# Kernel tuning notes

Measured on AMD Instinct MI355X. Metric: run time of the kernel, lower is better.

## Reference

```python
import jax, jax.numpy as jnp
import numpy as np
from jax import lax

L, B, D = 512, 128, 512   # listener frames, batch, listener feature dim
T, E, C, H, V = 200, 384, 128, 512, 46  # decode steps, embed, context, hidden(=E+C), vocab


def setup_inputs() -> dict:
    key = jax.random.key(0)
    ks = jax.random.split(key, 32)
    def p(i, shape, s=0.02):
        return jax.random.normal(ks[i], shape, dtype=jnp.float32) * s
    return {
        "listener_features": jax.random.normal(ks[0], (L, B, D), dtype=jnp.float32),
        "utterance_lengths": jax.random.randint(ks[1], (B,), L // 2, L + 1),
        "transcript": jax.random.randint(ks[2], (T, B), 0, V),
        "embedding": p(3, (V, E), 1.0),
        "w_ih0": p(4, (4 * H, E + C)), "w_hh0": p(5, (4 * H, H)),
        "b_ih0": jnp.zeros((4 * H,), jnp.float32), "b_hh0": jnp.zeros((4 * H,), jnp.float32),
        "w_ih1": p(6, (4 * H, H)), "w_hh1": p(7, (4 * H, H)),
        "b_ih1": jnp.zeros((4 * H,), jnp.float32), "b_hh1": jnp.zeros((4 * H,), jnp.float32),
        "w_ih2": p(8, (4 * H, H)), "w_hh2": p(9, (4 * H, H)),
        "b_ih2": jnp.zeros((4 * H,), jnp.float32), "b_hh2": jnp.zeros((4 * H,), jnp.float32),
        "phi_w": p(10, (C, H)), "phi_b": jnp.zeros((C,), jnp.float32),
        "key_w": p(11, (C, D)), "key_b": jnp.zeros((C,), jnp.float32),
        "value_w": p(12, (C, D)), "value_b": jnp.zeros((C,), jnp.float32),
        "out_w": p(13, (V, H + C)), "out_b": jnp.zeros((V,), jnp.float32),
        "init_hx0": jnp.zeros((1, H), jnp.float32), "init_cx0": jnp.zeros((1, H), jnp.float32),
        "init_hx1": jnp.zeros((1, H), jnp.float32), "init_cx1": jnp.zeros((1, H), jnp.float32),
        "init_hx2": jnp.zeros((1, H), jnp.float32), "init_cx2": jnp.zeros((1, H), jnp.float32),
    }


def _lstm_cell(x, h, c, w_ih, w_hh, b_ih, b_hh):
    gates = x @ w_ih.T + b_ih + h @ w_hh.T + b_hh  # [B,4H]
    i, f, g, o = jnp.split(gates, 4, axis=-1)
    c2 = jax.nn.sigmoid(f) * c + jax.nn.sigmoid(i) * jnp.tanh(g)
    h2 = jax.nn.sigmoid(o) * jnp.tanh(c2)
    return h2, c2


def reference(listener_features, utterance_lengths, transcript, embedding,
              w_ih0, w_hh0, b_ih0, b_hh0, w_ih1, w_hh1, b_ih1, b_hh1,
              w_ih2, w_hh2, b_ih2, b_hh2, phi_w, phi_b, key_w, key_b,
              value_w, value_b, out_w, out_b,
              init_hx0, init_cx0, init_hx1, init_cx1, init_hx2, init_cx2):
    nL, nB = listener_features.shape[0], listener_features.shape[1]
    mask = (jnp.arange(nL)[None, :] < utterance_lengths[:, None]).astype(jnp.float32)  # [B,L]
    # key/value projections are step-invariant (original recomputes them each step; same math)
    keyf = jnp.einsum('lbd,cd->blc', listener_features, key_w) + key_b   # [B,L,C]
    valf = jnp.einsum('lbd,cd->blc', listener_features, value_w) + value_b  # [B,L,C]

    def attend(hx2):
        q = hx2 @ phi_w.T + phi_b                      # [B,C]
        energy = jnp.einsum('bc,blc->bl', q, keyf)     # [B,L]
        a = jax.nn.softmax(energy, axis=-1) * mask
        a = a / jnp.maximum(jnp.sum(a, axis=-1, keepdims=True), 1e-12)  # F.normalize(p=1)
        ctx = jnp.einsum('bl,blc->bc', a, valf)        # [B,C]
        return a, ctx

    hx0 = jnp.broadcast_to(init_hx0, (nB, H)); cx0 = jnp.broadcast_to(init_cx0, (nB, H))
    hx1 = jnp.broadcast_to(init_hx1, (nB, H)); cx1 = jnp.broadcast_to(init_cx1, (nB, H))
    hx2 = jnp.broadcast_to(init_hx2, (nB, H)); cx2 = jnp.broadcast_to(init_cx2, (nB, H))
    _, ctx = attend(hx2)  # initial context from initial decoder state

    # teacher forcing: step t consumes <sos>(=0) then transcript[t-1]
    in_chars = jnp.concatenate([jnp.zeros((1, nB), transcript.dtype), transcript[:-1]], axis=0)  # [T,B]
    emb = embedding[in_chars]  # [T,B,E]

    def step(carry, emb_t):
        hx0, cx0, hx1, cx1, hx2, cx2, ctx = carry
        x = jnp.concatenate([emb_t, ctx], axis=-1)  # [B,E+C]
        hx0, cx0 = _lstm_cell(x, hx0, cx0, w_ih0, w_hh0, b_ih0, b_hh0)
        hx1, cx1 = _lstm_cell(hx0, hx1, cx1, w_ih1, w_hh1, b_ih1, b_hh1)
        hx2, cx2 = _lstm_cell(hx1, hx2, cx2, w_ih2, w_hh2, b_ih2, b_hh2)
        a, ctx = attend(hx2)
        logits = jnp.concatenate([hx2, ctx], axis=-1) @ out_w.T + out_b  # [B,V]
        return (hx0, cx0, hx1, cx1, hx2, cx2, ctx), (logits, a)

    carry0 = (hx0, cx0, hx1, cx1, hx2, cx2, ctx)
    _, (logits, attn) = lax.scan(step, carry0, emb)
    return logits, attn  # [T,B,V], [T,B,L]
```

## Files before the change

### kernel.cpp

```cpp
#include <hip/hip_runtime.h>

typedef unsigned short UST;
typedef unsigned int uint32;
typedef float f32x4 __attribute__((ext_vector_type(4)));
typedef short s16x8 __attribute__((ext_vector_type(8)));


__device__ __forceinline__ float b2f(UST u) {
  uint32 x = ((uint32)u) << 16;
  union { uint32 u; float f; } v; v.u = x; return v.f;
}
__device__ __forceinline__ UST f2bf(float f) {
  union { float f; uint32 u; } v; v.f = f;
  uint32 r = (v.u + 0x7fffu + ((v.u >> 16) & 1u)) >> 16;
  return (UST)r;
}
__device__ __forceinline__ ushort4 f2bf4(float4 v) {
  ushort4 r; r.x = f2bf(v.x); r.y = f2bf(v.y); r.z = f2bf(v.z); r.w = f2bf(v.w); return r;
}
__device__ __forceinline__ float sigf(float x) { return 1.f / (1.f + __expf(-x)); }
__device__ __forceinline__ float tanhf_(float x) { return 2.f / (1.f + __expf(-2.f * x)) - 1.f; }

union U8 { unsigned long long u; ushort4 s; uint2 w; };

__device__ __forceinline__ void st_flag(int* p, int v) {
  __hip_atomic_store(p, v, __ATOMIC_RELAXED, __HIP_MEMORY_SCOPE_AGENT);
}
__device__ __forceinline__ int ld_flag(const int* p) {
  return __hip_atomic_load(p, __ATOMIC_RELAXED, __HIP_MEMORY_SCOPE_AGENT);
}
__device__ __forceinline__ unsigned long long ld8(const void* p) {
  return __hip_atomic_load((const unsigned long long*)p, __ATOMIC_RELAXED, __HIP_MEMORY_SCOPE_AGENT);
}
__device__ __forceinline__ void st4(void* p, uint32 v) {
  __hip_atomic_store((uint32*)p, v, __ATOMIC_RELAXED, __HIP_MEMORY_SCOPE_AGENT);
}
__device__ __forceinline__ uint4 ld16c(const UST* p) {
  U8 a, b; a.u = ld8(p); b.u = ld8(p + 4);
  uint4 v; v.x = a.w.x; v.y = a.w.y; v.z = b.w.x; v.w = b.w.y; return v;
}

__device__ __forceinline__ void signal_flag(int* fl, int idx, int val, int tid) {
  __atomic_signal_fence(__ATOMIC_SEQ_CST);
  __builtin_amdgcn_s_waitcnt(0);
  __atomic_signal_fence(__ATOMIC_SEQ_CST);
  __syncthreads();
  if (tid == 0) st_flag(&fl[idx * 16], val);
}
__device__ __forceinline__ void wait128f(int* fl, int val, int tid, unsigned long long dl) {
  if (tid < 128) {
    while (ld_flag(&fl[tid * 16]) < val) {
      if (__builtin_amdgcn_s_memrealtime() > dl) break;
      __builtin_amdgcn_s_sleep(1);
    }
  }
  __syncthreads();
}
__device__ __forceinline__ void wait64f(int* fl, int val, int tid, unsigned long long dl) {
  if (tid < 64) {
    while (ld_flag(&fl[tid * 16]) < val) {
      if (__builtin_amdgcn_s_memrealtime() > dl) break;
      __builtin_amdgcn_s_sleep(1);
    }
  }
  __syncthreads();
}

struct Args {
  const float* lf; const int* ulen; const int* tr; const float* emb;
  const float* wih0; const float* whh0; const float* bih0; const float* bhh0;
  const float* wih1; const float* whh1; const float* bih1; const float* bhh1;
  const float* wih2; const float* whh2; const float* bih2; const float* bhh2;
  const float* phi_w; const float* phi_b; const float* key_w; const float* key_b;
  const float* val_w; const float* val_b; const float* out_w; const float* out_b;
  const float* ihx0; const float* icx0; const float* ihx1; const float* icx1;
  const float* ihx2; const float* icx2;
  int* bar; UST* wr; UST* xemb; UST* phi_bf; UST* keyfT; UST* valfT;
  UST* hx0; UST* hx1; UST* hx2; UST* ctx; UST* h2h; UST* cxh;
  float* out_logits; float* out_attn;
};

__global__ void __launch_bounds__(256) kprep(Args A) {
  const long N0 = 8192;
  const long N1 = 3L * 2048 * 1024;
  const long N2 = 200L * 128 * 384;
  const long N3 = 128L * 512;
  long total = N0 + N1 + N2 + N3;
  long stride = (long)gridDim.x * blockDim.x;
  for (long ii = (long)blockIdx.x * 256 + threadIdx.x; ii < total; ii += stride) {
    long j = ii;
    if (j < N0) { A.bar[j] = 0; continue; }
    j -= N0;
    if (j < N1) {
      int q = (int)j;
      int i = q & 7, lane = (q >> 3) & 63, nt = (q >> 9) & 1, ks = (q >> 10) & 31;
      int js = (q >> 15) & 63, cell = q >> 21;
      int gr = js * 32 + nt * 16 + (lane & 15);
      int jc = gr >> 2, g = gr & 3, k = ks * 32 + (lane >> 4) * 8 + i;
      const float* wi = cell == 0 ? A.wih0 : cell == 1 ? A.wih1 : A.wih2;
      const float* wh = cell == 0 ? A.whh0 : cell == 1 ? A.whh1 : A.whh2;
      float v;
      if (cell == 0)
        v = (k < 384) ? wi[(g * 512 + jc) * 512 + k]
          : (k < 896) ? wh[(g * 512 + jc) * 512 + k - 384]
                      : wi[(g * 512 + jc) * 512 + k - 512];
      else
        v = (k < 512) ? wi[(g * 512 + jc) * 512 + k] : wh[(g * 512 + jc) * 512 + k - 512];
      A.wr[j] = f2bf(v);
      continue;
    }
    j -= N1;
    if (j < N2) {
      int t = (int)(j / 49152); int r = (int)(j % 49152); int bb = r / 384; int e = r - bb * 384;
      int ch = (t == 0) ? 0 : A.tr[(t - 1) * 128 + bb];
      A.xemb[j] = f2bf(A.emb[ch * 384 + e]);
      continue;
    }
    j -= N2;
    A.phi_bf[j] = f2bf(A.phi_w[j]);
  }
}

__global__ void __launch_bounds__(256) kkv(Args A) {
  __shared__ __attribute__((aligned(16))) char sm[17408 + 34816];
  UST (*A_lds)[136] = (UST(*)[136])sm;
  UST (*W_lds)[136] = (UST(*)[136])(sm + 17408);
  float* sbuf = (float*)(sm + 17408);
  int tid = threadIdx.x, lane = tid & 63, wv = tid >> 6, ln = lane & 15, qd = lane >> 4;
  int blk = blockIdx.x;
  int b = blk >> 4, lt = (blk >> 1) & 7, kv = blk & 1;
  int l0 = lt * 64;
  const float* W = kv ? A.val_w : A.key_w;
  const float* bs = kv ? A.val_b : A.key_b;
  UST* outp = kv ? A.valfT : A.keyfT;
  f32x4 acc[8];
#pragma unroll
  for (int nt = 0; nt < 8; ++nt) {
    float x = bs[nt * 16 + ln];
    f32x4 t; t[0] = x; t[1] = x; t[2] = x; t[3] = x; acc[nt] = t;
  }
  for (int cc = 0; cc < 4; ++cc) {
    int d0 = cc * 128;
#pragma unroll
    for (int it = 0; it < 8; ++it) {
      int idx = it * 256 + tid, row = idx >> 5, seg = idx & 31;
      float4 v = *(const float4*)(A.lf + ((size_t)(l0 + row) * 128 + b) * 512 + d0 + seg * 4);
      *(ushort4*)&A_lds[row][seg * 4] = f2bf4(v);
    }
#pragma unroll
    for (int it = 0; it < 16; ++it) {
      int idx = it * 256 + tid, row = idx >> 5, seg = idx & 31;
      float4 v = *(const float4*)(W + (size_t)row * 512 + d0 + seg * 4);
      *(ushort4*)&W_lds[row][seg * 4] = f2bf4(v);
    }
    __syncthreads();
#pragma unroll
    for (int ks = 0; ks < 4; ++ks) {
      s16x8 av = *(const s16x8*)&A_lds[wv * 16 + ln][ks * 32 + qd * 8];
#pragma unroll
      for (int nt = 0; nt < 8; ++nt) {
        s16x8 bv = *(const s16x8*)&W_lds[nt * 16 + ln][ks * 32 + qd * 8];
        acc[nt] = __builtin_amdgcn_mfma_f32_16x16x32_bf16(av, bv, acc[nt], 0, 0, 0);
      }
    }
    __syncthreads();
  }
#pragma unroll
  for (int nt = 0; nt < 8; ++nt)
#pragma unroll
    for (int r = 0; r < 4; ++r)
      sbuf[(wv * 16 + qd * 4 + r) * 128 + nt * 16 + ln] = acc[nt][r];
  __syncthreads();
  int c2 = tid >> 1, lh = tid & 1;
  for (int g8 = 0; g8 < 4; ++g8) {
    UST tmp[8];
#pragma unroll
    for (int i = 0; i < 8; ++i) tmp[i] = f2bf(sbuf[(lh * 32 + g8 * 8 + i) * 128 + c2]);
    *(uint4*)(outp + ((size_t)b * 128 + c2) * 512 + l0 + lh * 32 + g8 * 8) = *(uint4*)tmp;
  }
}

__device__ __forceinline__ void stage_plain(int cS, int rB, const UST* src, UST (*X)[512]) {
  uint4 rg[16];
#pragma unroll
  for (int it = 0; it < 16; ++it)
    rg[it] = ld16c(src + (it * 4 + rB) * 512 + cS * 8);
  __syncthreads();
#pragma unroll
  for (int it = 0; it < 16; ++it) {
    int r = it * 4 + rB;
    *(uint4*)&X[r][(cS ^ (r & 7)) * 8] = rg[it];
  }
  __syncthreads();
}
__device__ __forceinline__ void compute_h(int w, int ln, int qd, int lane,
    const UST* wb, int h, UST (*X)[512], f32x4 acc[4][2]) {
#pragma unroll
  for (int j = 0; j < 4; ++j) {
    int ls = w * 4 + j;
    int ksg = h * 16 + ls;
    s16x8 b0 = *(const s16x8*)(wb + ((size_t)(ksg * 2 + 0) * 64 + lane) * 8);
    s16x8 b1 = *(const s16x8*)(wb + ((size_t)(ksg * 2 + 1) * 64 + lane) * 8);
#pragma unroll
    for (int rt = 0; rt < 4; ++rt) {
      int r = rt * 16 + ln, c = ls * 4 + qd;
      s16x8 av = *(const s16x8*)&X[r][(c ^ (r & 7)) * 8];
      acc[rt][0] = __builtin_amdgcn_mfma_f32_16x16x32_bf16(av, b0, acc[rt][0], 0, 0, 0);
      acc[rt][1] = __builtin_amdgcn_mfma_f32_16x16x32_bf16(av, b1, acc[rt][1], 0, 0, 0);
    }
  }
}
__device__ __forceinline__ void zacc(f32x4 acc[4][2]) {
#pragma unroll
  for (int rt = 0; rt < 4; ++rt)
#pragma unroll
    for (int nt = 0; nt < 2; ++nt) {
      acc[rt][nt][0] = 0.f; acc[rt][nt][1] = 0.f; acc[rt][nt][2] = 0.f; acc[rt][nt][3] = 0.f;
    }
}
__device__ __forceinline__ void cell_epilogue(const Args& A, int cell, int t, int m, int j0,
    int tid, int w, int ln, int qd, f32x4 acc[4][2], float* FB,
    const float* bias8, float* cr, UST* hdst) {
  __syncthreads();
#pragma unroll
  for (int rt = 0; rt < 4; ++rt)
#pragma unroll
    for (int nt = 0; nt < 2; ++nt)
#pragma unroll
      for (int reg = 0; reg < 4; ++reg)
        FB[w * 2112 + (rt * 16 + qd * 4 + reg) * 33 + nt * 16 + ln] = acc[rt][nt][reg];
  __syncthreads();
  int row = tid >> 2, q4 = tid & 3, grow = m * 64 + row;
  uint32 upack = 0;
#pragma unroll
  for (int jj = 0; jj < 2; ++jj) {
    int gc = (q4 * 2 + jj) * 4;
    int o = row * 33 + gc;
    float g0 = FB[o] + FB[2112 + o] + FB[4224 + o] + FB[6336 + o] + bias8[jj * 4 + 0];
    float g1 = FB[o + 1] + FB[2112 + o + 1] + FB[4224 + o + 1] + FB[6336 + o + 1] + bias8[jj * 4 + 1];
    float g2 = FB[o + 2] + FB[2112 + o + 2] + FB[4224 + o + 2] + FB[6336 + o + 2] + bias8[jj * 4 + 2];
    float g3 = FB[o + 3] + FB[2112 + o + 3] + FB[4224 + o + 3] + FB[6336 + o + 3] + bias8[jj * 4 + 3];
    float cn = sigf(g1) * cr[jj] + sigf(g0) * tanhf_(g2);
    float hv = sigf(g3) * tanhf_(cn);
    cr[jj] = cn;
    upack |= ((uint32)f2bf(hv)) << (16 * jj);
  }
  st4(hdst + grow * 512 + j0 + q4 * 2, upack);
  if (cell == 2) *(uint32*)(A.h2h + ((size_t)t * 128 + grow) * 512 + j0 + q4 * 2) = upack;
}

__device__ void attend_f(const Args& A, int t, int p, int b, int tid, int lane, int wv,
                         char* smraw) {
  float* att_h = (float*)smraw;
  float* att_q = att_h + 512;
  float* att_c = att_q + 256;
  float* att_red = att_c + 128;
  float (*e_part)[512] = (float(*)[512])(att_red + 16);
  const UST* hx2p = A.hx2 + p * 65536;
  if (tid < 128) {
    U8 v; v.u = ld8(hx2p + b * 512 + tid * 4);
    att_h[tid * 4 + 0] = b2f(v.s.x); att_h[tid * 4 + 1] = b2f(v.s.y);
    att_h[tid * 4 + 2] = b2f(v.s.z); att_h[tid * 4 + 3] = b2f(v.s.w);
  }
  __syncthreads();
  int c = tid & 127, half = tid >> 7;
  {
    float acc = half ? 0.f : A.phi_b[c];
    const UST* pr = A.phi_bf + c * 512 + half * 256;
    const float* hh = att_h + half * 256;
#pragma unroll 4
    for (int k = 0; k < 256; k += 8) {
      uint4 v = *(const uint4*)(pr + k);
      const UST* us = (const UST*)&v;
#pragma unroll
      for (int i = 0; i < 8; ++i) acc += b2f(us[i]) * hh[k + i];
    }
    att_q[tid] = acc;
  }
  __syncthreads();
  if (tid < 128) att_q[tid] += att_q[tid + 128];
  __syncthreads();
  {
    int cg = tid >> 6, lg = tid & 63;
    float ep[8] = {0, 0, 0, 0, 0, 0, 0, 0};
    const UST* kb = A.keyfT + (size_t)b * 65536 + lg * 8;
#pragma unroll 4
    for (int c2 = cg * 32; c2 < cg * 32 + 32; ++c2) {
      uint4 v = *(const uint4*)(kb + (size_t)c2 * 512);
      const UST* us = (const UST*)&v;
      float qv = att_q[c2];
#pragma unroll
      for (int i = 0; i < 8; ++i) ep[i] += qv * b2f(us[i]);
    }
#pragma unroll
    for (int i = 0; i < 8; ++i) e_part[cg][lg * 8 + i] = ep[i];
  }
  __syncthreads();
  float e0 = e_part[0][2 * tid] + e_part[1][2 * tid] + e_part[2][2 * tid] + e_part[3][2 * tid];
  float e1 = e_part[0][2 * tid + 1] + e_part[1][2 * tid + 1] + e_part[2][2 * tid + 1] + e_part[3][2 * tid + 1];
  float mx = fmaxf(e0, e1);
#pragma unroll
  for (int off = 32; off; off >>= 1) mx = fmaxf(mx, __shfl_xor(mx, off));
  if (lane == 0) att_red[wv] = mx;
  __syncthreads();
  mx = fmaxf(fmaxf(att_red[0], att_red[1]), fmaxf(att_red[2], att_red[3]));
  int len = A.ulen[b];
  float x0 = (2 * tid < len) ? __expf(e0 - mx) : 0.f;
  float x1 = (2 * tid + 1 < len) ? __expf(e1 - mx) : 0.f;
  float s = x0 + x1;
#pragma unroll
  for (int off = 32; off; off >>= 1) s += __shfl_xor(s, off);
  if (lane == 0) att_red[8 + wv] = s;
  __syncthreads();
  s = att_red[8] + att_red[9] + att_red[10] + att_red[11];
  float inv = 1.f / fmaxf(s, 1e-12f);
  float a0 = x0 * inv, a1 = x1 * inv;
  float* esm = &e_part[0][0];
  esm[2 * tid] = a0; esm[2 * tid + 1] = a1;
  if (t >= 0) {
    float2 st; st.x = a0; st.y = a1;
    *(float2*)(A.out_attn + ((size_t)t * 128 + b) * 512 + 2 * tid) = st;
  }
  __syncthreads();
  {
    float acc = 0.f;
    const UST* vb = A.valfT + (size_t)b * 65536 + (size_t)c * 512 + half * 256;
    const float* aa = esm + half * 256;
#pragma unroll 4
    for (int k = 0; k < 256; k += 8) {
      uint4 v = *(const uint4*)(vb + k);
      const UST* us = (const UST*)&v;
#pragma unroll
      for (int i = 0; i < 8; ++i) acc += aa[k + i] * b2f(us[i]);
    }
    att_q[tid] = acc;
  }
  __syncthreads();
  if (tid < 128) att_c[tid] = att_q[tid] + att_q[tid + 128];
  __syncthreads();
  if (tid < 64) {
    float cv0 = att_c[2 * tid], cv1 = att_c[2 * tid + 1];
    uint32 u = (uint32)f2bf(cv0) | ((uint32)f2bf(cv1) << 16);
    st4(A.ctx + p * 16384 + b * 128 + 2 * tid, u);
    if (t >= 0) *(uint32*)(A.cxh + ((size_t)t * 128 + b) * 128 + 2 * tid) = u;
  }
}

__global__ void __launch_bounds__(256) kmain(Args A) {
  __shared__ __attribute__((aligned(16))) char smraw[65536];
  unsigned long long dl = __builtin_amdgcn_s_memrealtime() + 100000000ull;
  int blk = blockIdx.x, tid = threadIdx.x;
  int lane = tid & 63, w = tid >> 6, ln = lane & 15, qd = lane >> 4;
  int* c0f = A.bar;
  int* c1f = A.bar + 2048;
  int* c2f = A.bar + 4096;
  int* attf = A.bar + 6144;
  if (blk < 128) {
    UST (*X)[512] = (UST(*)[512])smraw;
    float* FB = (float*)smraw;
    int js = ((blk >> 4) << 3) | (blk & 7);
    int m = (blk >> 3) & 1;
    int j0 = js * 8;
    int sid = m * 64 + js;
    int* mc0 = c0f + m * 1024;
    int* mc1 = c1f + m * 1024;
    int* mat = attf + m * 1024;
    int cS = tid & 63, rB = tid >> 6;
    float bias[3][8]; float cr[3][2];
    {
      const float* bihA[3] = {A.bih0, A.bih1, A.bih2};
      const float* bhhA[3] = {A.bhh0, A.bhh1, A.bhh2};
      const float* icxA[3] = {A.icx0, A.icx1, A.icx2};
      const float* ihxA[3] = {A.ihx0, A.ihx1, A.ihx2};
      UST* hxA[3] = {A.hx0, A.hx1, A.hx2};
      int q4 = tid & 3;
#pragma unroll
      for (int cI = 0; cI < 3; ++cI) {
#pragma unroll
        for (int jj = 0; jj < 2; ++jj) {
          int col = j0 + q4 * 2 + jj;
          for (int g = 0; g < 4; ++g)
            bias[cI][jj * 4 + g] = bihA[cI][g * 512 + col] + bhhA[cI][g * 512 + col];
          cr[cI][jj] = icxA[cI][col];
        }
        int row = tid >> 2, grow = m * 64 + row, col0 = j0 + q4 * 2;
        uint32 u = (uint32)f2bf(ihxA[cI][col0]) | ((uint32)f2bf(ihxA[cI][col0 + 1]) << 16);
        st4(hxA[cI] + 65536 + grow * 512 + col0, u);
      }
    }
    signal_flag(c2f, sid, 1, tid);
    wait128f(c2f, 1, tid, dl);
    const UST* wrj = A.wr + (size_t)js * 32768;
    f32x4 acc[4][2];
    for (int t = 0; t < 200; ++t) {
      int p = t & 1, po = p ^ 1;
      const UST* xe = A.xemb + (size_t)t * 49152 + m * 64 * 384;
      const UST* h0r = A.hx0 + po * 65536 + m * 64 * 512;
      const UST* h1r = A.hx1 + po * 65536 + m * 64 * 512;
      const UST* h2r = A.hx2 + po * 65536 + m * 64 * 512;
      const UST* cxr = A.ctx + po * 16384 + m * 64 * 128;
      zacc(acc);
      {
        uint4 rg[16];
        if (cS < 48) {
#pragma unroll
          for (int it = 0; it < 16; ++it)
            rg[it] = *(const uint4*)(xe + (it * 4 + rB) * 384 + cS * 8);
        } else {
#pragma unroll
          for (int it = 0; it < 16; ++it)
            rg[it] = ld16c(h0r + (it * 4 + rB) * 512 + (cS - 48) * 8);
        }
        __syncthreads();
#pragma unroll
        for (int it = 0; it < 16; ++it) {
          int r = it * 4 + rB;
          *(uint4*)&X[r][(cS ^ (r & 7)) * 8] = rg[it];
        }
        __syncthreads();
      }
      compute_h(w, ln, qd, lane, wrj, 0, X, acc);
      {
        uint4 rg[16];
        if (cS < 48) {
#pragma unroll
          for (int it = 0; it < 16; ++it)
            rg[it] = ld16c(h0r + (it * 4 + rB) * 512 + (cS + 16) * 8);
        }
        wait64f(mat, t + 1, tid, dl);
        if (cS >= 48) {
#pragma unroll
          for (int it = 0; it < 16; ++it)
            rg[it] = ld16c(cxr + (it * 4 + rB) * 128 + (cS - 48) * 8);
        }
#pragma unroll
        for (int it = 0; it < 16; ++it) {
          int r = it * 4 + rB;
          *(uint4*)&X[r][(cS ^ (r & 7)) * 8] = rg[it];
        }
        __syncthreads();
      }
      compute_h(w, ln, qd, lane, wrj, 1, X, acc);
      cell_epilogue(A, 0, t, m, j0, tid, w, ln, qd, acc, FB, bias[0], cr[0], A.hx0 + p * 65536);
      signal_flag(c0f, sid, t + 2, tid);
      const UST* h0n = A.hx0 + p * 65536 + m * 64 * 512;
      zacc(acc);
      stage_plain(cS, rB, h1r, X);
      compute_h(w, ln, qd, lane, wrj + 2097152, 1, X, acc);
      wait64f(mc0, t + 2, tid, dl);
      stage_plain(cS, rB, h0n, X);
      compute_h(w, ln, qd, lane, wrj + 2097152, 0, X, acc);
      cell_epilogue(A, 1, t, m, j0, tid, w, ln, qd, acc, FB, bias[1], cr[1], A.hx1 + p * 65536);
      signal_flag(c1f, sid, t + 2, tid);
      const UST* h1n = A.hx1 + p * 65536 + m * 64 * 512;
      zacc(acc);
      stage_plain(cS, rB, h2r, X);
      compute_h(w, ln, qd, lane, wrj + 4194304, 1, X, acc);
      wait64f(mc1, t + 2, tid, dl);
      stage_plain(cS, rB, h1n, X);
      compute_h(w, ln, qd, lane, wrj + 4194304, 0, X, acc);
      cell_epilogue(A, 2, t, m, j0, tid, w, ln, qd, acc, FB, bias[2], cr[2], A.hx2 + p * 65536);
      signal_flag(c2f, sid, t + 2, tid);
    }
  } else {
    int b = blk - 128;
    int* mc2a = c2f + (b >> 6) * 1024;
    wait128f(c2f, 1, tid, dl);
    attend_f(A, -1, 1, b, tid, lane, w, smraw);
    signal_flag(attf, b, 1, tid);
    for (int t = 0; t < 200; ++t) {
      wait64f(mc2a, t + 2, tid, dl);
      attend_f(A, t, t & 1, b, tid, lane, w, smraw);
      signal_flag(attf, b, t + 2, tid);
    }
  }
}

__global__ void __launch_bounds__(256) kepi(Args A) {
  __shared__ UST ow[46 * 648];
  __shared__ float ob[46];
  int t = blockIdx.x, tid = threadIdx.x;
  for (int i = tid; i < 46 * 640; i += 256) {
    int v = i / 640, k = i - v * 640; ow[v * 648 + k] = f2bf(A.out_w[i]);
  }
  if (tid < 46) ob[tid] = A.out_b[tid];
  __syncthreads();
  for (int oi = tid; oi < 128 * 46; oi += 256) {
    int bb = oi / 46, v = oi - bb * 46;
    const UST* xh = A.h2h + ((size_t)t * 128 + bb) * 512;
    const UST* xc = A.cxh + ((size_t)t * 128 + bb) * 128;
    const UST* wrow = &ow[v * 648];
    float acc = ob[v];
    for (int k = 0; k < 512; k += 8) {
      uint4 xv = *(const uint4*)(xh + k);
      uint4 wv4 = *(const uint4*)(wrow + k);
      const UST* xs = (const UST*)&xv; const UST* wl = (const UST*)&wv4;
#pragma unroll
      for (int i = 0; i < 8; ++i) acc += b2f(xs[i]) * b2f(wl[i]);
    }
    for (int k = 0; k < 128; k += 8) {
      uint4 xv = *(const uint4*)(xc + k);
      uint4 wv4 = *(const uint4*)(wrow + 512 + k);
      const UST* xs = (const UST*)&xv; const UST* wl = (const UST*)&wv4;
#pragma unroll
      for (int i = 0; i < 8; ++i) acc += b2f(xs[i]) * b2f(wl[i]);
    }
    A.out_logits[((size_t)t * 128 + bb) * 46 + v] = acc;
  }
}

extern "C" void kernel_launch(void* const* d_in, const int* in_sizes, int n_in,
                              void* d_out, int out_size, void* d_ws, size_t ws_size,
                              hipStream_t stream) {
  (void)in_sizes; (void)n_in; (void)out_size; (void)ws_size;
  Args a;
  a.lf = (const float*)d_in[0]; a.ulen = (const int*)d_in[1]; a.tr = (const int*)d_in[2];
  a.emb = (const float*)d_in[3];
  a.wih0 = (const float*)d_in[4]; a.whh0 = (const float*)d_in[5]; a.bih0 = (const float*)d_in[6]; a.bhh0 = (const float*)d_in[7];
  a.wih1 = (const float*)d_in[8]; a.whh1 = (const float*)d_in[9]; a.bih1 = (const float*)d_in[10]; a.bhh1 = (const float*)d_in[11];
  a.wih2 = (const float*)d_in[12]; a.whh2 = (const float*)d_in[13]; a.bih2 = (const float*)d_in[14]; a.bhh2 = (const float*)d_in[15];
  a.phi_w = (const float*)d_in[16]; a.phi_b = (const float*)d_in[17];
  a.key_w = (const float*)d_in[18]; a.key_b = (const float*)d_in[19];
  a.val_w = (const float*)d_in[20]; a.val_b = (const float*)d_in[21];
  a.out_w = (const float*)d_in[22]; a.out_b = (const float*)d_in[23];
  a.ihx0 = (const float*)d_in[24]; a.icx0 = (const float*)d_in[25];
  a.ihx1 = (const float*)d_in[26]; a.icx1 = (const float*)d_in[27];
  a.ihx2 = (const float*)d_in[28]; a.icx2 = (const float*)d_in[29];
  char* ws = (char*)d_ws;
  a.bar    = (int*)ws;
  a.wr     = (UST*)(ws + 32768);
  a.xemb   = (UST*)(ws + 12615680);
  a.phi_bf = (UST*)(ws + 32276480);
  a.keyfT  = (UST*)(ws + 32407552);
  a.valfT  = (UST*)(ws + 49184768);
  a.hx0    = (UST*)(ws + 65961984);
  a.hx1    = (UST*)(ws + 66224128);
  a.hx2    = (UST*)(ws + 66486272);
  a.ctx    = (UST*)(ws + 66748416);
  a.h2h    = (UST*)(ws + 66813952);
  a.cxh    = (UST*)(ws + 93028352);
  a.out_logits = (float*)d_out;
  a.out_attn   = (float*)d_out + 1177600;
  kprep<<<4096, 256, 0, stream>>>(a);
  kkv<<<2048, 256, 0, stream>>>(a);
  kmain<<<256, 256, 0, stream>>>(a);
  kepi<<<200, 256, 0, stream>>>(a);
}
```

Measured before the change: 7.339 ms.

## Reorder LSTM step to hoist recurrent GEMMs off critical path; register-cache attention keys/values

The LSTM worker blocks now compute the recurrent (h_prev) contributions for all three cells early in each step, using separate accumulators. Only the input-side products that depend on freshly produced h0/h1/context are left on the cross-block dependency chain. The context contribution is split off so the wait on attention happens as late as possible. Attention blocks preload their per-batch key and value slices into registers once, instead of re-reading them from global memory every step. The cost is higher register pressure, which may hurt occupancy or cause spills.

```diff
diff --git a/kernel.cpp b/kernel.cpp
--- a/kernel.cpp
+++ b/kernel.cpp
@@ -193,17 +193,18 @@
   }
   __syncthreads();
 }
-__device__ __forceinline__ void compute_h(int w, int ln, int qd, int lane,
-    const UST* wb, int h, UST (*X)[512], f32x4 acc[4][2]) {
-#pragma unroll
-  for (int j = 0; j < 4; ++j) {
-    int ls = w * 4 + j;
-    int ksg = h * 16 + ls;
+template <int SPW>
+__device__ __forceinline__ void compute_r(int w, int ln, int qd, int lane,
+    const UST* wb, int ksgBase, int chunkBase, UST (*X)[512], f32x4 acc[4][2]) {
+#pragma unroll
+  for (int j = 0; j < SPW; ++j) {
+    int ls = w * SPW + j;
+    int ksg = ksgBase + ls;
     s16x8 b0 = *(const s16x8*)(wb + ((size_t)(ksg * 2 + 0) * 64 + lane) * 8);
     s16x8 b1 = *(const s16x8*)(wb + ((size_t)(ksg * 2 + 1) * 64 + lane) * 8);
 #pragma unroll
     for (int rt = 0; rt < 4; ++rt) {
-      int r = rt * 16 + ln, c = ls * 4 + qd;
+      int r = rt * 16 + ln, c = chunkBase + ls * 4 + qd;
       s16x8 av = *(const s16x8*)&X[r][(c ^ (r & 7)) * 8];
       acc[rt][0] = __builtin_amdgcn_mfma_f32_16x16x32_bf16(av, b0, acc[rt][0], 0, 0, 0);
       acc[rt][1] = __builtin_amdgcn_mfma_f32_16x16x32_bf16(av, b1, acc[rt][1], 0, 0, 0);
@@ -249,8 +250,8 @@
   if (cell == 2) *(uint32*)(A.h2h + ((size_t)t * 128 + grow) * 512 + j0 + q4 * 2) = upack;
 }
 
-__device__ void attend_f(const Args& A, int t, int p, int b, int tid, int lane, int wv,
-                         char* smraw) {
+__device__ __forceinline__ void attend_f(const Args& A, int t, int p, int b, int tid,
+    int lane, int wv, char* smraw, const uint4 (&rgK)[32], const uint4 (&rgV)[32]) {
   float* att_h = (float*)smraw;
   float* att_q = att_h + 512;
   float* att_c = att_q + 256;
@@ -283,14 +284,12 @@
   {
     int cg = tid >> 6, lg = tid & 63;
     float ep[8] = {0, 0, 0, 0, 0, 0, 0, 0};
-    const UST* kb = A.keyfT + (size_t)b * 65536 + lg * 8;
-#pragma unroll 4
-    for (int c2 = cg * 32; c2 < cg * 32 + 32; ++c2) {
-      uint4 v = *(const uint4*)(kb + (size_t)c2 * 512);
-      const UST* us = (const UST*)&v;
-      float qv = att_q[c2];
-#pragma unroll
-      for (int i = 0; i < 8; ++i) ep[i] += qv * b2f(us[i]);
+#pragma unroll
+    for (int i = 0; i < 32; ++i) {
+      float qv = att_q[cg * 32 + i];
+      const UST* us = (const UST*)&rgK[i];
+#pragma unroll
+      for (int j = 0; j < 8; ++j) ep[j] += qv * b2f(us[j]);
     }
 #pragma unroll
     for (int i = 0; i < 8; ++i) e_part[cg][lg * 8 + i] = ep[i];
@@ -324,14 +323,12 @@
   __syncthreads();
   {
     float acc = 0.f;
-    const UST* vb = A.valfT + (size_t)b * 65536 + (size_t)c * 512 + half * 256;
     const float* aa = esm + half * 256;
-#pragma unroll 4
-    for (int k = 0; k < 256; k += 8) {
-      uint4 v = *(const uint4*)(vb + k);
-      const UST* us = (const UST*)&v;
-#pragma unroll
-      for (int i = 0; i < 8; ++i) acc += aa[k + i] * b2f(us[i]);
+#pragma unroll
+    for (int i = 0; i < 32; ++i) {
+      const UST* us = (const UST*)&rgV[i];
+#pragma unroll
+      for (int j = 0; j < 8; ++j) acc += aa[i * 8 + j] * b2f(us[j]);
     }
     att_q[tid] = acc;
   }
@@ -364,6 +361,7 @@
     int sid = m * 64 + js;
     int* mc0 = c0f + m * 1024;
     int* mc1 = c1f + m * 1024;
+    int* mc2 = c2f + m * 1024;
     int* mat = attf + m * 1024;
     int cS = tid & 63, rB = tid >> 6;
     float bias[3][8]; float cr[3][2];
@@ -390,8 +388,10 @@
     }
     signal_flag(c2f, sid, 1, tid);
     wait128f(c2f, 1, tid, dl);
-    const UST* wrj = A.wr + (size_t)js * 32768;
-    f32x4 acc[4][2];
+    const UST* wrj0 = A.wr + (size_t)js * 32768;
+    const UST* wrj1 = wrj0 + 2097152;
+    const UST* wrj2 = wrj0 + 4194304;
+    f32x4 acc0[4][2], acc1[4][2], acc2[4][2];
     for (int t = 0; t < 200; ++t) {
       int p = t & 1, po = p ^ 1;
       const UST* xe = A.xemb + (size_t)t * 49152 + m * 64 * 384;
@@ -399,7 +399,7 @@
       const UST* h1r = A.hx1 + po * 65536 + m * 64 * 512;
       const UST* h2r = A.hx2 + po * 65536 + m * 64 * 512;
       const UST* cxr = A.ctx + po * 16384 + m * 64 * 128;
-      zacc(acc);
+      zacc(acc0); zacc(acc1); zacc(acc2);
       {
         uint4 rg[16];
         if (cS < 48) {
@@ -419,7 +419,7 @@
         }
         __syncthreads();
       }
-      compute_h(w, ln, qd, lane, wrj, 0, X, acc);
+      compute_r<4>(w, ln, qd, lane, wrj0, 0, 0, X, acc0);
       {
         uint4 rg[16];
         if (cS < 48) {
@@ -427,50 +427,75 @@
           for (int it = 0; it < 16; ++it)
             rg[it] = ld16c(h0r + (it * 4 + rB) * 512 + (cS + 16) * 8);
         }
-        wait64f(mat, t + 1, tid, dl);
-        if (cS >= 48) {
-#pragma unroll
-          for (int it = 0; it < 16; ++it)
-            rg[it] = ld16c(cxr + (it * 4 + rB) * 128 + (cS - 48) * 8);
-        }
-#pragma unroll
-        for (int it = 0; it < 16; ++it) {
-          int r = it * 4 + rB;
-          *(uint4*)&X[r][(cS ^ (r & 7)) * 8] = rg[it];
+        __syncthreads();
+        if (cS < 48) {
+#pragma unroll
+          for (int it = 0; it < 16; ++it) {
+            int r = it * 4 + rB;
+            *(uint4*)&X[r][(cS ^ (r & 7)) * 8] = rg[it];
+          }
         }
         __syncthreads();
       }
-      compute_h(w, ln, qd, lane, wrj, 1, X, acc);
-      cell_epilogue(A, 0, t, m, j0, tid, w, ln, qd, acc, FB, bias[0], cr[0], A.hx0 + p * 65536);
+      compute_r<3>(w, ln, qd, lane, wrj0, 16, 0, X, acc0);
+      stage_plain(cS, rB, h1r, X);
+      compute_r<4>(w, ln, qd, lane, wrj1, 16, 0, X, acc1);
+      wait64f(mc2, t + 1, tid, dl);
+      stage_plain(cS, rB, h2r, X);
+      compute_r<4>(w, ln, qd, lane, wrj2, 16, 0, X, acc2);
+      wait64f(mat, t + 1, tid, dl);
+      {
+        uint4 rg[16];
+        if (cS >= 48) {
+#pragma unroll
+          for (int it = 0; it < 16; ++it)
+            rg[it] = ld16c(cxr + (it * 4 + rB) * 128 + (cS - 48) * 8);
+#pragma unroll
+          for (int it = 0; it < 16; ++it) {
+            int r = it * 4 + rB;
+            *(uint4*)&X[r][(cS ^ (r & 7)) * 8] = rg[it];
+          }
+        }
+        __syncthreads();
+      }
+      compute_r<1>(w, ln, qd, lane, wrj0, 28, 48, X, acc0);
+      cell_epilogue(A, 0, t, m, j0, tid, w, ln, qd, acc0, FB, bias[0], cr[0], A.hx0 + p * 65536);
       signal_flag(c0f, sid, t + 2, tid);
       const UST* h0n = A.hx0 + p * 65536 + m * 64 * 512;
-      zacc(acc);
-      stage_plain(cS, rB, h1r, X);
-      compute_h(w, ln, qd, lane, wrj + 2097152, 1, X, acc);
       wait64f(mc0, t + 2, tid, dl);
       stage_plain(cS, rB, h0n, X);
-      compute_h(w, ln, qd, lane, wrj + 2097152, 0, X, acc);
-      cell_epilogue(A, 1, t, m, j0, tid, w, ln, qd, acc, FB, bias[1], cr[1], A.hx1 + p * 65536);
+      compute_r<4>(w, ln, qd, lane, wrj1, 0, 0, X, acc1);
+      cell_epilogue(A, 1, t, m, j0, tid, w, ln, qd, acc1, FB, bias[1], cr[1], A.hx1 + p * 65536);
       signal_flag(c1f, sid, t + 2, tid);
       const UST* h1n = A.hx1 + p * 65536 + m * 64 * 512;
-      zacc(acc);
-      stage_plain(cS, rB, h2r, X);
-      compute_h(w, ln, qd, lane, wrj + 4194304, 1, X, acc);
       wait64f(mc1, t + 2, tid, dl);
       stage_plain(cS, rB, h1n, X);
-      compute_h(w, ln, qd, lane, wrj + 4194304, 0, X, acc);
-      cell_epilogue(A, 2, t, m, j0, tid, w, ln, qd, acc, FB, bias[2], cr[2], A.hx2 + p * 65536);
+      compute_r<4>(w, ln, qd, lane, wrj2, 0, 0, X, acc2);
+      cell_epilogue(A, 2, t, m, j0, tid, w, ln, qd, acc2, FB, bias[2], cr[2], A.hx2 + p * 65536);
       signal_flag(c2f, sid, t + 2, tid);
     }
   } else {
     int b = blk - 128;
     int* mc2a = c2f + (b >> 6) * 1024;
+    uint4 rgK[32], rgV[32];
+    {
+      int cg = tid >> 6, lg = tid & 63;
+      const UST* kb = A.keyfT + (size_t)b * 65536 + lg * 8;
+#pragma unroll
+      for (int i = 0; i < 32; ++i)
+        rgK[i] = *(const uint4*)(kb + (size_t)(cg * 32 + i) * 512);
+      int c = tid & 127, half = tid >> 7;
+      const UST* vb = A.valfT + (size_t)b * 65536 + (size_t)c * 512 + half * 256;
+#pragma unroll
+      for (int i = 0; i < 32; ++i)
+        rgV[i] = *(const uint4*)(vb + i * 8);
+    }
     wait128f(c2f, 1, tid, dl);
-    attend_f(A, -1, 1, b, tid, lane, w, smraw);
+    attend_f(A, -1, 1, b, tid, lane, w, smraw, rgK, rgV);
     signal_flag(attf, b, 1, tid);
     for (int t = 0; t < 200; ++t) {
       wait64f(mc2a, t + 2, tid, dl);
-      attend_f(A, t, t & 1, b, tid, lane, w, smraw);
+      attend_f(A, t, t & 1, b, tid, lane, w, smraw, rgK, rgV);
       signal_flag(attf, b, t + 2, tid);
     }
   }
```

Result: no change. 7.196 ms (-1.9%).
